# Optimization experiments

Measured on AMD Instinct MI355X. Metric: run time of the kernel, lower is better.

Reference implementation:

```python
import jax, jax.numpy as jnp
import numpy as np

BLOCK = 9      # photometric_loss block size
LOSS_EPS = 0.5 # census ternary threshold


def _sign_eps(d, eps):
    # ternary census: -1 / 0 / +1 with dead-zone eps
    return jnp.where(d < -eps, -1.0, jnp.where(d > eps, 1.0, 0.0))


def _census_sad(es, ta, block, eps):
    # per-pixel mean over valid 9x9 window of |census(es) - census(ta)|
    B, C, H, W = es.shape
    P = block // 2
    pad = ((0, 0), (0, 0), (P, P), (P, P))
    esp = jnp.pad(es, pad)
    tap = jnp.pad(ta, pad)
    vp = jnp.pad(jnp.ones((1, 1, H, W), es.dtype), pad)  # validity of shifted px
    total = jnp.zeros_like(es)
    count = jnp.zeros((1, 1, H, W), es.dtype)
    for dh in range(-P, P + 1):          # fixed 9x9 structural loop
        for dw in range(-P, P + 1):
            es_s = esp[:, :, P + dh:P + dh + H, P + dw:P + dw + W]
            ta_s = tap[:, :, P + dh:P + dh + H, P + dw:P + dw + W]
            v = vp[:, :, P + dh:P + dh + H, P + dw:P + dw + W]
            c = jnp.abs(_sign_eps(es_s - es, eps) - _sign_eps(ta_s - ta, eps))
            total = total + v * c
            count = count + v
    return total / count


def reference(disp0, im, pattern):
    B, _, H, W = disp0.shape
    # pattern.mean(dim=1, keepdim=True)
    pat = jnp.broadcast_to(pattern.mean(axis=1, keepdims=True), (B, 1, H, W))
    # grid_sample(align_corners=True, border) with y unchanged reduces to
    # clamped 1D linear interpolation along width at x = u - disp
    u = jnp.arange(W, dtype=disp0.dtype)
    x = jnp.clip(u[None, None, None, :] - disp0, 0.0, W - 1)  # [B,1,H,W]
    x0 = jnp.floor(x).astype(jnp.int32)
    x1 = jnp.minimum(x0 + 1, W - 1)
    w = x - x0.astype(x.dtype)
    p0 = jnp.take_along_axis(pat, x0, axis=3)
    p1 = jnp.take_along_axis(pat, x1, axis=3)
    pattern_proj = p0 * (1.0 - w) + p1 * w
    diff = _census_sad(pattern_proj, im, BLOCK, LOSS_EPS)
    # mask = ones (std=None): (mask*diff).sum()/mask.sum() == mean
    val = diff.mean()
    return val, pattern_proj


def setup_inputs() -> dict:
    key = jax.random.key(0)
    k1, k2, k3 = jax.random.split(key, 3)
    B, H, W = 16, 512, 640
    disp0 = jax.random.uniform(k1, (B, 1, H, W), dtype=jnp.float32) * 64.0
    im = jax.random.uniform(k2, (B, 1, H, W), dtype=jnp.float32)
    pattern = jax.random.uniform(k3, (1, 3, H, W), dtype=jnp.float32)
    return {"disp0": disp0, "im": im, "pattern": pattern}
```

## Files before the change

kernel.cpp:

```cpp
#include <hip/hip_runtime.h>

#define BB 16
#define HH 512
#define WW 640
constexpr int HW = HH * WW;

#define WT 64
#define HT 16
#define RP 4
#define PAD 4
#define LW (WT + 2*PAD)
#define LH (HT + PAD)
#define LHW (LH * LW)
#define NIT ((LHW + 255) / 256)
#define GX (WW / WT)
#define GY (HH / HT)
#define NBLK (GX * GY * BB)

constexpr float HALO = 1.0e6f;

__device__ __forceinline__ float fast_rcp(float x) {
    return __builtin_amdgcn_rcpf(x);
}

__global__ __launch_bounds__(256)
void pm_kernel(const float* __restrict__ pattern, float* __restrict__ pm)
{
    int i = blockIdx.x * 256 + threadIdx.x;
    if (i < HW)
        pm[i] = (pattern[i] + pattern[HW + i] + pattern[2 * HW + i]) * (1.0f / 3.0f);
}

__global__ __launch_bounds__(256)
void interior_kernel(const float* __restrict__ disp0,
                     const float* __restrict__ im,
                     const float* __restrict__ pm,
                     float* __restrict__ out,
                     float* __restrict__ partial)
{
    __shared__ float2 sm[LHW];
    __shared__ int wsum[4];

    const int bx = blockIdx.x + 1;
    const int by = blockIdx.y + 1;
    const int b  = blockIdx.z;
    const int tx = threadIdx.x, rg = threadIdx.y;
    const int tid = rg * 64 + tx;

    const float* db = disp0 + (size_t)b * HW;
    const float* ib = im    + (size_t)b * HW;
    float* proj = out + 1 + (size_t)b * HW;

    const int gh0 = by * HT;
    const int gw0 = bx * WT - PAD;

    float dv[NIT], tv[NIT];
    #pragma unroll
    for (int it = 0; it < NIT; ++it) {
        int i = tid + it * 256;
        if (i < LHW) {
            int lh = i / LW, lw = i - lh * LW;
            int g = (gh0 + lh) * WW + (gw0 + lw);
            dv[it] = db[g];
            tv[it] = ib[g];
        }
    }
    #pragma unroll
    for (int it = 0; it < NIT; ++it) {
        int i = tid + it * 256;
        if (i < LHW) {
            int lh = i / LW, lw = i - lh * LW;
            int gh = gh0 + lh, gw = gw0 + lw;
            int g = gh * WW + gw;
            float x = fminf(fmaxf((float)gw - dv[it], 0.0f), (float)(WW - 1));
            int   x0 = (int)x;
            int   x1 = min(x0 + 1, WW - 1);
            float w  = x - (float)x0;
            const float* pr = pm + gh * WW;
            float ev = pr[x0] * (1.0f - w) + pr[x1] * w;
            if ((lh < HT) & (lw >= PAD) & (lw < PAD + WT))
                proj[g] = ev;
            sm[i] = make_float2(ev, tv[it]);
        }
    }
    __syncthreads();

    float ehi[RP], elo[RP], thi[RP], tlo[RP];
    #pragma unroll
    for (int p = 0; p < RP; ++p) {
        float2 c = sm[(rg * RP + p) * LW + tx + PAD];
        ehi[p] = c.x + 0.5f;  elo[p] = c.x - 0.5f;
        thi[p] = c.y + 0.5f;  tlo[p] = c.y - 0.5f;
    }
    int acc[RP] = {0, 0, 0, 0};
    #pragma unroll
    for (int wr = 0; wr < RP + PAD; ++wr) {
        const float2* row = sm + (rg * RP + wr) * LW + tx;
        float2 v[9];
        #pragma unroll
        for (int j = 0; j < 9; ++j) v[j] = row[j];
        #pragma unroll
        for (int p = 0; p < RP; ++p) {
            int dh = wr - p;
            if (dh == 0) {
                #pragma unroll
                for (int j = 5; j <= 8; ++j) {
                    acc[p] += (int)((v[j].x > ehi[p]) != (v[j].y > thi[p]));
                    acc[p] += (int)((v[j].x < elo[p]) != (v[j].y < tlo[p]));
                }
            } else if (dh >= 1 && dh <= PAD) {
                #pragma unroll
                for (int j = 0; j <= 8; ++j) {
                    acc[p] += (int)((v[j].x > ehi[p]) != (v[j].y > thi[p]));
                    acc[p] += (int)((v[j].x < elo[p]) != (v[j].y < tlo[p]));
                }
            }
        }
    }
    int a = (acc[0] + acc[1]) + (acc[2] + acc[3]);
    #pragma unroll
    for (int off = 32; off > 0; off >>= 1)
        a += __shfl_down(a, off, 64);
    if (tx == 0) wsum[rg] = a;
    __syncthreads();
    if (tid == 0)
        partial[(b * GY + by) * GX + bx] =
            (float)(wsum[0] + wsum[1] + wsum[2] + wsum[3]) * (2.0f / 81.0f);
}

__global__ __launch_bounds__(256)
void edge_kernel(const float* __restrict__ disp0,
                 const float* __restrict__ im,
                 const float* __restrict__ pm,
                 float* __restrict__ out,
                 float* __restrict__ partial)
{
    const int bx = blockIdx.x, by = blockIdx.y, b = blockIdx.z;
    if ((bx >= 1) & (bx <= GX - 2) & (by >= 1) & (by <= GY - 2)) return;

    __shared__ float2 sm[LHW];
    __shared__ float wsumf[4];

    const int tx = threadIdx.x, rg = threadIdx.y;
    const int tid = rg * 64 + tx;

    const float* db = disp0 + (size_t)b * HW;
    const float* ib = im    + (size_t)b * HW;
    float* proj = out + 1 + (size_t)b * HW;

    const int gh0 = by * HT;
    const int gw0 = bx * WT - PAD;

    #pragma unroll
    for (int it = 0; it < NIT; ++it) {
        int i = tid + it * 256;
        if (i < LHW) {
            int lh = i / LW, lw = i - lh * LW;
            int gh = gh0 + lh, gw = gw0 + lw;
            float ev = HALO, tv = HALO;
            if ((gh < HH) & (gw >= 0) & (gw < WW)) {
                int g = gh * WW + gw;
                float d = db[g];
                float x = fminf(fmaxf((float)gw - d, 0.0f), (float)(WW - 1));
                int   x0 = (int)x;
                int   x1 = min(x0 + 1, WW - 1);
                float w  = x - (float)x0;
                const float* pr = pm + gh * WW;
                ev = pr[x0] * (1.0f - w) + pr[x1] * w;
                tv = ib[g];
                if ((lh < HT) & (lw >= PAD) & (lw < PAD + WT))
                    proj[g] = ev;
            }
            sm[i] = make_float2(ev, tv);
        }
    }
    __syncthreads();

    float invcw[9];
    const int w0 = bx * WT + tx;
    #pragma unroll
    for (int j = 0; j < 9; ++j) {
        int c  = w0 + j - PAD;
        int cw = min(PAD, WW - 1 - c) + min(PAD, c) + 1;
        invcw[j] = fast_rcp((float)cw);
    }

    float ehi[RP], elo[RP], thi[RP], tlo[RP], wp[RP], facc[RP];
    int iacc[RP];
    #pragma unroll
    for (int p = 0; p < RP; ++p) {
        float2 c = sm[(rg * RP + p) * LW + tx + PAD];
        ehi[p] = c.x + 0.5f;  elo[p] = c.x - 0.5f;
        thi[p] = c.y + 0.5f;  tlo[p] = c.y - 0.5f;
        int r  = by * HT + rg * RP + p;
        int ch = min(PAD, HH - 1 - r) + min(PAD, r) + 1;
        wp[p]  = fast_rcp((float)ch) * invcw[PAD];
        facc[p] = 0.0f;
        iacc[p] = 0;
    }

    #pragma unroll
    for (int wr = 0; wr < RP + PAD; ++wr) {
        int r  = by * HT + rg * RP + wr;
        int ch = min(PAD, HH - 1 - r) + min(PAD, r) + 1;
        float rowinv = fast_rcp((float)ch);

        const float2* row = sm + (rg * RP + wr) * LW + tx;
        float2 v[9];
        #pragma unroll
        for (int j = 0; j < 9; ++j) v[j] = row[j];

        #pragma unroll
        for (int p = 0; p < RP; ++p) {
            const bool d0 = (p == wr);
            if (p <= wr && p >= wr - PAD) {
                #pragma unroll
                for (int j = 0; j <= 8; ++j) {
                    if (d0 && j <= 4) continue;
                    int bh = (int)((v[j].x > ehi[p]) != (v[j].y > thi[p]));
                    int bl = (int)((v[j].x < elo[p]) != (v[j].y < tlo[p]));
                    int c  = bh + bl;
                    facc[p] = fmaf((float)c, rowinv * invcw[j], facc[p]);
                    iacc[p] += c;
                }
            }
        }
    }
    float tsum = 0.0f;
    #pragma unroll
    for (int p = 0; p < RP; ++p)
        tsum += facc[p] + wp[p] * (float)iacc[p];

    #pragma unroll
    for (int off = 32; off > 0; off >>= 1)
        tsum += __shfl_down(tsum, off, 64);
    if (tx == 0) wsumf[rg] = tsum;
    __syncthreads();
    if (tid == 0)
        partial[(b * GY + by) * GX + bx] = wsumf[0] + wsumf[1] + wsumf[2] + wsumf[3];
}

__global__ __launch_bounds__(256)
void reduce_kernel(const float* __restrict__ partial, float* __restrict__ out)
{
    __shared__ float wsum[4];
    int t = threadIdx.x;
    float s = 0.0f;
    #pragma unroll
    for (int i = 0; i < NBLK / 256; ++i) s += partial[t + i * 256];
    #pragma unroll
    for (int off = 32; off > 0; off >>= 1)
        s += __shfl_down(s, off, 64);
    if ((t & 63) == 0) wsum[t >> 6] = s;
    __syncthreads();
    if (t == 0)
        out[0] = (wsum[0] + wsum[1] + wsum[2] + wsum[3]) * (1.0f / ((float)BB * (float)HW));
}

extern "C" void kernel_launch(void* const* d_in, const int* in_sizes, int n_in,
                              void* d_out, int out_size, void* d_ws, size_t ws_size,
                              hipStream_t stream) {
    const float* disp0   = (const float*)d_in[0];
    const float* im      = (const float*)d_in[1];
    const float* pattern = (const float*)d_in[2];
    float* out = (float*)d_out;
    float* pm      = (float*)d_ws;
    float* partial = pm + HW;

    pm_kernel<<<(HW + 255) / 256, 256, 0, stream>>>(pattern, pm);

    dim3 block(64, 4);
    dim3 gridI(GX - 2, GY - 2, BB);
    interior_kernel<<<gridI, block, 0, stream>>>(disp0, im, pm, out, partial);

    dim3 gridE(GX, GY, BB);
    edge_kernel<<<gridE, block, 0, stream>>>(disp0, im, pm, out, partial);

    reduce_kernel<<<1, 256, 0, stream>>>(partial, out);
}
```

Measured before the change: 173.1 us.

## Fuse pattern mean into gather, use scalar-mask census counting and atomic reduction

Drops the separate pattern-mean kernel and averages the three pattern channels inside the gather, so each sample now does six loads instead of two. The census comparisons become inline asm that compares across the wavefront, XORs the masks and popcounts them into one scalar accumulator, so no cross-lane shuffle reduction is needed. The partial-sum buffer and reduce kernel are replaced by per-wave float atomicAdd into the output, plus a zero kernel at the start. The edge kernel's grid is shrunk to exactly the 80 border tiles per image, so the early-return blocks are no longer launched. Costs: more pattern loads, summation order that is not deterministic, and inline asm tied to wave64.

```diff
diff --git a/kernel.cpp b/kernel.cpp
--- a/kernel.cpp
+++ b/kernel.cpp
@@ -15,31 +15,47 @@
 #define NIT ((LHW + 255) / 256)
 #define GX (WW / WT)
 #define GY (HH / HT)
-#define NBLK (GX * GY * BB)
-
-constexpr float HALO = 1.0e6f;
+
+constexpr float HALO  = 1.0e6f;
+constexpr float INV_N = 1.0f / (16.0f * 327680.0f);
+constexpr float K_INT = (2.0f / 81.0f) * INV_N;
 
 __device__ __forceinline__ float fast_rcp(float x) {
     return __builtin_amdgcn_rcpf(x);
 }
 
-__global__ __launch_bounds__(256)
-void pm_kernel(const float* __restrict__ pattern, float* __restrict__ pm)
+__device__ __forceinline__ void tap_scalar(float ex, float tq, float eh, float th,
+                                           float el, float tl, int& acc)
 {
-    int i = blockIdx.x * 256 + threadIdx.x;
-    if (i < HW)
-        pm[i] = (pattern[i] + pattern[HW + i] + pattern[2 * HW + i]) * (1.0f / 3.0f);
-}
+    unsigned long long m1, m2;
+    int c1, c2;
+    asm("v_cmp_gt_f32 %[m1], %[ex], %[eh]\n\t"
+        "v_cmp_gt_f32 %[m2], %[tq], %[th]\n\t"
+        "s_xor_b64 %[m1], %[m1], %[m2]\n\t"
+        "s_bcnt1_i32_b64 %[c1], %[m1]\n\t"
+        "v_cmp_lt_f32 %[m1], %[ex], %[el]\n\t"
+        "v_cmp_lt_f32 %[m2], %[tq], %[tl]\n\t"
+        "s_xor_b64 %[m1], %[m1], %[m2]\n\t"
+        "s_bcnt1_i32_b64 %[c2], %[m1]\n\t"
+        "s_add_i32 %[acc], %[acc], %[c1]\n\t"
+        "s_add_i32 %[acc], %[acc], %[c2]"
+        : [m1]"=&s"(m1), [m2]"=&s"(m2), [c1]"=&s"(c1), [c2]"=&s"(c2),
+          [acc]"+s"(acc)
+        : [ex]"v"(ex), [tq]"v"(tq), [eh]"v"(eh), [th]"v"(th),
+          [el]"v"(el), [tl]"v"(tl)
+        : "scc");
+}
+
+__global__ __launch_bounds__(1)
+void zero_kernel(float* __restrict__ out) { out[0] = 0.0f; }
 
 __global__ __launch_bounds__(256)
 void interior_kernel(const float* __restrict__ disp0,
                      const float* __restrict__ im,
-                     const float* __restrict__ pm,
-                     float* __restrict__ out,
-                     float* __restrict__ partial)
+                     const float* __restrict__ pattern,
+                     float* __restrict__ out)
 {
     __shared__ float2 sm[LHW];
-    __shared__ int wsum[4];
 
     const int bx = blockIdx.x + 1;
     const int by = blockIdx.y + 1;
@@ -76,8 +92,10 @@
             int   x0 = (int)x;
             int   x1 = min(x0 + 1, WW - 1);
             float w  = x - (float)x0;
-            const float* pr = pm + gh * WW;
-            float ev = pr[x0] * (1.0f - w) + pr[x1] * w;
+            const float* pr = pattern + gh * WW;
+            float p0 = (pr[x0] + pr[HW + x0] + pr[2*HW + x0]) * (1.0f/3.0f);
+            float p1 = (pr[x1] + pr[HW + x1] + pr[2*HW + x1]) * (1.0f/3.0f);
+            float ev = p0 * (1.0f - w) + p1 * w;
             if ((lh < HT) & (lw >= PAD) & (lw < PAD + WT))
                 proj[g] = ev;
             sm[i] = make_float2(ev, tv[it]);
@@ -92,7 +110,7 @@
         ehi[p] = c.x + 0.5f;  elo[p] = c.x - 0.5f;
         thi[p] = c.y + 0.5f;  tlo[p] = c.y - 0.5f;
     }
-    int acc[RP] = {0, 0, 0, 0};
+    int acc = 0;
     #pragma unroll
     for (int wr = 0; wr < RP + PAD; ++wr) {
         const float2* row = sm + (rg * RP + wr) * LW + tx;
@@ -104,43 +122,32 @@
             int dh = wr - p;
             if (dh == 0) {
                 #pragma unroll
-                for (int j = 5; j <= 8; ++j) {
-                    acc[p] += (int)((v[j].x > ehi[p]) != (v[j].y > thi[p]));
-                    acc[p] += (int)((v[j].x < elo[p]) != (v[j].y < tlo[p]));
-                }
+                for (int j = 5; j <= 8; ++j)
+                    tap_scalar(v[j].x, v[j].y, ehi[p], thi[p], elo[p], tlo[p], acc);
             } else if (dh >= 1 && dh <= PAD) {
                 #pragma unroll
-                for (int j = 0; j <= 8; ++j) {
-                    acc[p] += (int)((v[j].x > ehi[p]) != (v[j].y > thi[p]));
-                    acc[p] += (int)((v[j].x < elo[p]) != (v[j].y < tlo[p]));
-                }
+                for (int j = 0; j <= 8; ++j)
+                    tap_scalar(v[j].x, v[j].y, ehi[p], thi[p], elo[p], tlo[p], acc);
             }
         }
     }
-    int a = (acc[0] + acc[1]) + (acc[2] + acc[3]);
-    #pragma unroll
-    for (int off = 32; off > 0; off >>= 1)
-        a += __shfl_down(a, off, 64);
-    if (tx == 0) wsum[rg] = a;
-    __syncthreads();
-    if (tid == 0)
-        partial[(b * GY + by) * GX + bx] =
-            (float)(wsum[0] + wsum[1] + wsum[2] + wsum[3]) * (2.0f / 81.0f);
+    if (tx == 0)
+        atomicAdd(out, (float)acc * K_INT);
 }
 
 __global__ __launch_bounds__(256)
 void edge_kernel(const float* __restrict__ disp0,
                  const float* __restrict__ im,
-                 const float* __restrict__ pm,
-                 float* __restrict__ out,
-                 float* __restrict__ partial)
+                 const float* __restrict__ pattern,
+                 float* __restrict__ out)
 {
-    const int bx = blockIdx.x, by = blockIdx.y, b = blockIdx.z;
-    if ((bx >= 1) & (bx <= GX - 2) & (by >= 1) & (by <= GY - 2)) return;
-
     __shared__ float2 sm[LHW];
-    __shared__ float wsumf[4];
-
+
+    const int t = blockIdx.x;
+    int bx, by;
+    if (t < 20) { by = (t >= 10) ? (GY - 1) : 0; bx = t % 10; }
+    else        { int s = t - 20; bx = (s & 1) * (GX - 1); by = 1 + (s >> 1); }
+    const int b  = blockIdx.y;
     const int tx = threadIdx.x, rg = threadIdx.y;
     const int tid = rg * 64 + tx;
 
@@ -165,8 +172,10 @@
                 int   x0 = (int)x;
                 int   x1 = min(x0 + 1, WW - 1);
                 float w  = x - (float)x0;
-                const float* pr = pm + gh * WW;
-                ev = pr[x0] * (1.0f - w) + pr[x1] * w;
+                const float* pr = pattern + gh * WW;
+                float p0 = (pr[x0] + pr[HW + x0] + pr[2*HW + x0]) * (1.0f/3.0f);
+                float p1 = (pr[x1] + pr[HW + x1] + pr[2*HW + x1]) * (1.0f/3.0f);
+                ev = p0 * (1.0f - w) + p1 * w;
                 tv = ib[g];
                 if ((lh < HT) & (lw >= PAD) & (lw < PAD + WT))
                     proj[g] = ev;
@@ -234,27 +243,8 @@
     #pragma unroll
     for (int off = 32; off > 0; off >>= 1)
         tsum += __shfl_down(tsum, off, 64);
-    if (tx == 0) wsumf[rg] = tsum;
-    __syncthreads();
-    if (tid == 0)
-        partial[(b * GY + by) * GX + bx] = wsumf[0] + wsumf[1] + wsumf[2] + wsumf[3];
-}
-
-__global__ __launch_bounds__(256)
-void reduce_kernel(const float* __restrict__ partial, float* __restrict__ out)
-{
-    __shared__ float wsum[4];
-    int t = threadIdx.x;
-    float s = 0.0f;
-    #pragma unroll
-    for (int i = 0; i < NBLK / 256; ++i) s += partial[t + i * 256];
-    #pragma unroll
-    for (int off = 32; off > 0; off >>= 1)
-        s += __shfl_down(s, off, 64);
-    if ((t & 63) == 0) wsum[t >> 6] = s;
-    __syncthreads();
-    if (t == 0)
-        out[0] = (wsum[0] + wsum[1] + wsum[2] + wsum[3]) * (1.0f / ((float)BB * (float)HW));
+    if (tx == 0)
+        atomicAdd(out, tsum * INV_N);
 }
 
 extern "C" void kernel_launch(void* const* d_in, const int* in_sizes, int n_in,
@@ -264,17 +254,13 @@
     const float* im      = (const float*)d_in[1];
     const float* pattern = (const float*)d_in[2];
     float* out = (float*)d_out;
-    float* pm      = (float*)d_ws;
-    float* partial = pm + HW;
-
-    pm_kernel<<<(HW + 255) / 256, 256, 0, stream>>>(pattern, pm);
+
+    zero_kernel<<<1, 1, 0, stream>>>(out);
 
     dim3 block(64, 4);
     dim3 gridI(GX - 2, GY - 2, BB);
-    interior_kernel<<<gridI, block, 0, stream>>>(disp0, im, pm, out, partial);
-
-    dim3 gridE(GX, GY, BB);
-    edge_kernel<<<gridE, block, 0, stream>>>(disp0, im, pm, out, partial);
-
-    reduce_kernel<<<1, 256, 0, stream>>>(partial, out);
-}
+    interior_kernel<<<gridI, block, 0, stream>>>(disp0, im, pattern, out);
+
+    dim3 gridE(80, BB);
+    edge_kernel<<<gridE, block, 0, stream>>>(disp0, im, pattern, out);
+}
```

Measured after the change: 378.6 us. 2.19x slower.
